# Kernel optimization log

Hardware: AMD Instinct MI355X
Metric: run time of the kernel (lower is better)

The kernel has to match this reference:

```python
import jax, jax.numpy as jnp
import numpy as np

B, S, DIM = 2, 2048, 2048
NH = 16
D_NOPE, D_ROPE, D_V = 128, 64, 128
D_QK = D_NOPE + D_ROPE  # 192
KV_RANK = 512
RMS_EPS = 1e-6


def setup_inputs() -> dict:
    key = jax.random.key(0)
    ks = jax.random.split(key, 8)
    x = jax.random.normal(ks[0], (B, S, DIM), dtype=jnp.float32)
    # rotary freqs as (cos, sin) pairs: [S, D_ROPE//2, 2]
    pos = jnp.arange(S, dtype=jnp.float32)
    inv_freq = 1.0 / (10000.0 ** (jnp.arange(0, D_ROPE, 2, dtype=jnp.float32) / D_ROPE))
    ang = pos[:, None] * inv_freq[None, :]
    freqs_cis = jnp.stack([jnp.cos(ang), jnp.sin(ang)], axis=-1)
    # causal mask [S, S]
    mask = jnp.where(jnp.arange(S)[None, :] > jnp.arange(S)[:, None], -jnp.inf, 0.0).astype(jnp.float32)
    sd = lambda k, shp, fan: jax.random.normal(k, shp, dtype=jnp.float32) * (fan ** -0.5)
    wq = sd(ks[1], (NH * D_QK, DIM), DIM)
    wkv_a = sd(ks[2], (KV_RANK + D_ROPE, DIM), DIM)
    wkv_b = sd(ks[3], (NH * (D_NOPE + D_V), KV_RANK), KV_RANK)
    wo = sd(ks[4], (DIM, NH * D_V), NH * D_V)
    kv_norm_w = jnp.ones((KV_RANK,), dtype=jnp.float32)
    return {"x": x, "start_pos": 0, "freqs_cis": freqs_cis, "mask": mask,
            "wq": wq, "wkv_a": wkv_a, "wkv_b": wkv_b, "wo": wo, "kv_norm_w": kv_norm_w}


def _rope(x, freqs):
    # x: [b, s, h, d] with d even; freqs: [s, d//2, 2] (cos, sin)
    b, s, h, d = x.shape
    xr = x.reshape(b, s, h, d // 2, 2)
    cos = freqs[None, :, None, :, 0]
    sin = freqs[None, :, None, :, 1]
    ye = xr[..., 0] * cos - xr[..., 1] * sin
    yo = xr[..., 0] * sin + xr[..., 1] * cos
    return jnp.stack([ye, yo], axis=-1).reshape(b, s, h, d)


def _rms_norm(x, w):
    var = jnp.mean(jnp.square(x), axis=-1, keepdims=True)
    return x * jax.lax.rsqrt(var + RMS_EPS) * w


def reference(x, start_pos, freqs_cis, mask, wq, wkv_a, wkv_b, wo, kv_norm_w):
    b, s, _ = x.shape
    scale = D_QK ** -0.5
    # query projection -> [b, s, h, d_qk]
    q = jnp.einsum('bsd,ed->bse', x, wq).reshape(b, s, NH, D_QK)
    q_nope, q_pe = q[..., :D_NOPE], q[..., D_NOPE:]
    q_pe = _rope(q_pe, freqs_cis)
    q = jnp.concatenate([q_nope, q_pe], axis=-1)
    # latent kv projection -> [b, s, kv_rank + d_rope]
    kv = jnp.einsum('bsd,ed->bse', x, wkv_a)
    kv_lat, k_pe = kv[..., :KV_RANK], kv[..., KV_RANK:]
    k_pe = _rope(k_pe[:, :, None, :], freqs_cis)  # [b, s, 1, d_rope]
    kv_up = jnp.einsum('bsr,er->bse', _rms_norm(kv_lat, kv_norm_w), wkv_b)
    kv_up = kv_up.reshape(b, s, NH, D_NOPE + D_V)
    k_nope, v = kv_up[..., :D_NOPE], kv_up[..., D_NOPE:]
    k = jnp.concatenate([k_nope, jnp.broadcast_to(k_pe, (b, s, NH, D_ROPE))], axis=-1)
    # start_pos = 0 prefill: cache[:end_pos] == freshly computed k, v
    scores = jnp.einsum('bshd,bthd->bsht', q, k) * scale
    if mask is not None:
        scores = scores + mask[None, :, None, :]
    probs = jax.nn.softmax(scores.astype(jnp.float32), axis=-1).astype(x.dtype)
    out = jnp.einsum('bsht,bthd->bshd', probs, v)
    return jnp.einsum('bse,de->bsd', out.reshape(b, s, NH * D_V), wo)
```

## Files before the change

### kernel.cpp

```cpp
#include <hip/hip_runtime.h>
#include <hip/hip_bf16.h>


typedef __bf16 bf16x8 __attribute__((ext_vector_type(8)));
typedef float  f32x4  __attribute__((ext_vector_type(4)));
typedef float  f32x16 __attribute__((ext_vector_type(16)));
typedef unsigned short us8 __attribute__((ext_vector_type(8)));
typedef unsigned short us4 __attribute__((ext_vector_type(4)));
typedef unsigned int   ui4 __attribute__((ext_vector_type(4)));

#define S_LEN   2048
#define BS_TOT  4096
#define NH      16
#define DQK     192
#define DV      128
#define KV_RANK 512
#define QSTR    3840

__device__ inline unsigned short f2bf(float f) {
  __hip_bfloat16 h = __float2bfloat16(f);
  return *reinterpret_cast<unsigned short*>(&h);
}
__device__ inline float bfu2f(unsigned short u) {
  unsigned int x = ((unsigned int)u) << 16;
  return __builtin_bit_cast(float, x);
}
__device__ inline unsigned int pack2bf(float a, float b) {
  return (unsigned int)f2bf(a) | ((unsigned int)f2bf(b) << 16);
}
__device__ inline void glds16(const void* g, void* l) {
  __builtin_amdgcn_global_load_lds(
      (const __attribute__((address_space(1))) unsigned int*)g,
      (__attribute__((address_space(3))) unsigned int*)l, 16, 0, 0);
}

__global__ __launch_bounds__(256) void cast_all_kernel(
    const float* __restrict__ x, const float* __restrict__ wq,
    const float* __restrict__ wkva, const float* __restrict__ wkvb,
    const float* __restrict__ wo,
    __hip_bfloat16* __restrict__ xb, __hip_bfloat16* __restrict__ wqb,
    __hip_bfloat16* __restrict__ wkvab, __hip_bfloat16* __restrict__ wkvbb,
    __hip_bfloat16* __restrict__ wob) {
  const int bid = blockIdx.x;
  const float* src; __hip_bfloat16* dst; int n, npad, b0, nb;
  if (bid < 771)       { src = x;    dst = xb;    n = 8388608; npad = 8388608; b0 = 0;    nb = 771; }
  else if (bid < 1349) { src = wq;   dst = wqb;   n = 6291456; npad = 6291456; b0 = 771;  nb = 578; }
  else if (bid < 1469) { src = wkva; dst = wkvab; n = 1179648; npad = 1572864; b0 = 1349; nb = 120; }
  else if (bid < 1662) { src = wkvb; dst = wkvbb; n = 2097152; npad = 2097152; b0 = 1469; nb = 193; }
  else                 { src = wo;   dst = wob;   n = 4194304; npad = 4194304; b0 = 1662; nb = 386; }
  const int tid = (bid - b0) * 256 + threadIdx.x;
  const int stride = nb * 256;
  for (int i = tid * 4; i < npad; i += stride * 4) {
    if (i + 3 < n) {
      f32x4 v = *(const f32x4*)(src + i);
      dst[i + 0] = __float2bfloat16(v.x);
      dst[i + 1] = __float2bfloat16(v.y);
      dst[i + 2] = __float2bfloat16(v.z);
      dst[i + 3] = __float2bfloat16(v.w);
    } else {
#pragma unroll
      for (int z = 0; z < 4; z++)
        dst[i + z] = __float2bfloat16((i + z < n) ? src[i + z] : 0.f);
    }
  }
}

template<int OUT_BF16>
__global__ __launch_bounds__(512, 2) void gemm_bt256(
    const __hip_bfloat16* __restrict__ A, const __hip_bfloat16* __restrict__ Bw,
    void* __restrict__ Cp, int M, int N, int K, int nbx) {
  __shared__ alignas(16) unsigned short Asl[2][256 * 64];
  __shared__ alignas(16) unsigned short Bsl[2][256 * 64];

  const int nwg = gridDim.x;
  const int cpx = nwg >> 3;
  const int id  = (blockIdx.x & 7) * cpx + (blockIdx.x >> 3);
  const int bx = id % nbx, by = id / nbx;
  const int m0 = by * 256, n0 = bx * 256;

  const int tid = threadIdx.x, w = tid >> 6, lane = tid & 63;
  const int wr = w >> 2, wc = w & 3;
  const int ml = lane & 15, quad = lane >> 4;
  const int srow = w * 8 + (lane >> 3);
  const int scol = ((lane & 7) ^ (lane >> 3)) * 8;

  const unsigned short* Ag = (const unsigned short*)A + (size_t)(m0 + srow) * K + scol;
  const unsigned short* Bg = (const unsigned short*)Bw + (size_t)(n0 + srow) * K + scol;

  f32x4 acc[8][4];
#pragma unroll
  for (int i = 0; i < 8; i++)
#pragma unroll
    for (int j = 0; j < 4; j++)
#pragma unroll
      for (int e = 0; e < 4; e++) acc[i][j][e] = 0.0f;

  auto stage = [&](int slot, int k0) {
#pragma unroll
    for (int j = 0; j < 4; j++)
      glds16(Ag + (size_t)j * 64 * K + k0, &Asl[slot][(j * 64 + w * 8) * 64]);
#pragma unroll
    for (int j = 0; j < 4; j++)
      glds16(Bg + (size_t)j * 64 * K + k0, &Bsl[slot][(j * 64 + w * 8) * 64]);
  };

  const int nt = K / 64;
  stage(0, 0);
  stage(1, 64);
  asm volatile("s_waitcnt vmcnt(8)" ::: "memory");
  __builtin_amdgcn_s_barrier();
  asm volatile("" ::: "memory");

  int slot = 0;
  for (int t = 0; t < nt; ++t) {
    const unsigned short* As = &Asl[slot][0];
    const unsigned short* Bs = &Bsl[slot][0];

    bf16x8 bfr[2][2][2];
#pragma unroll
    for (int nh = 0; nh < 2; nh++)
#pragma unroll
      for (int nf = 0; nf < 2; nf++) {
        int r = wc * 64 + nh * 32 + nf * 16 + ml;
        const char* rowp = (const char*)&Bs[r * 64];
#pragma unroll
        for (int ks = 0; ks < 2; ks++)
          bfr[nh][nf][ks] =
              *(const bf16x8*)(rowp + ((ks * 64 + quad * 16) ^ ((ml & 7) << 4)));
      }
#pragma unroll
    for (int mh = 0; mh < 2; mh++) {
      bf16x8 af[4][2];
#pragma unroll
      for (int mf = 0; mf < 4; mf++) {
        int r = wr * 128 + mh * 64 + mf * 16 + ml;
        const char* rowp = (const char*)&As[r * 64];
#pragma unroll
        for (int ks = 0; ks < 2; ks++)
          af[mf][ks] =
              *(const bf16x8*)(rowp + ((ks * 64 + quad * 16) ^ ((ml & 7) << 4)));
      }
      __builtin_amdgcn_s_setprio(1);
#pragma unroll
      for (int nh = 0; nh < 2; nh++)
#pragma unroll
        for (int mf = 0; mf < 4; mf++)
#pragma unroll
          for (int nf = 0; nf < 2; nf++)
#pragma unroll
            for (int ks = 0; ks < 2; ks++)
              acc[mh * 4 + mf][nh * 2 + nf] = __builtin_amdgcn_mfma_f32_16x16x32_bf16(
                  af[mf][ks], bfr[nh][nf][ks], acc[mh * 4 + mf][nh * 2 + nf], 0, 0, 0);
      __builtin_amdgcn_s_setprio(0);
    }

    asm volatile("" ::: "memory");
    __builtin_amdgcn_s_barrier();
    asm volatile("" ::: "memory");
    if (t + 2 < nt) {
      stage(slot, (t + 2) * 64);
      asm volatile("s_waitcnt vmcnt(8)" ::: "memory");
    } else {
      asm volatile("s_waitcnt vmcnt(0)" ::: "memory");
    }
    __builtin_amdgcn_s_barrier();
    asm volatile("" ::: "memory");
    slot ^= 1;
  }

#pragma unroll
  for (int mi = 0; mi < 8; mi++) {
#pragma unroll
    for (int ni = 0; ni < 4; ni++) {
      int col = n0 + wc * 64 + ni * 16 + ml;
      int rowb = m0 + wr * 128 + mi * 16 + quad * 4;
#pragma unroll
      for (int j = 0; j < 4; j++) {
        float v = acc[mi][ni][j];
        if (OUT_BF16)
          ((__hip_bfloat16*)Cp)[(size_t)(rowb + j) * N + col] = __float2bfloat16(v);
        else
          ((float*)Cp)[(size_t)(rowb + j) * N + col] = v;
      }
    }
  }
}

__global__ __launch_bounds__(256) void rope_rms_kernel(
    __hip_bfloat16* __restrict__ qkv, const float* __restrict__ w,
    const float* __restrict__ freqs, __hip_bfloat16* __restrict__ latent,
    __hip_bfloat16* __restrict__ kpe_out) {
  int si = blockIdx.x;
  int s  = si & (S_LEN - 1);
  int tid = threadIdx.x;
#pragma unroll
  for (int p = tid; p < NH * 32; p += 256) {
    int h = p >> 5, i = p & 31;
    size_t base = (size_t)si * QSTR + h * DQK + 128 + 2 * i;
    float c  = freqs[s * 64 + 2 * i];
    float sn = freqs[s * 64 + 2 * i + 1];
    float x0 = __bfloat162float(qkv[base]);
    float x1 = __bfloat162float(qkv[base + 1]);
    qkv[base]     = __float2bfloat16(x0 * c - x1 * sn);
    qkv[base + 1] = __float2bfloat16(x0 * sn + x1 * c);
  }
  const unsigned short* row = (const unsigned short*)qkv + (size_t)si * QSTR + 3072;
  float v0 = bfu2f(row[tid]), v1 = bfu2f(row[tid + 256]);
  float ss = v0 * v0 + v1 * v1;
#pragma unroll
  for (int off = 1; off < 64; off <<= 1) ss += __shfl_xor(ss, off, 64);
  __shared__ float red[4];
  if ((tid & 63) == 0) red[tid >> 6] = ss;
  __syncthreads();
  float tot = red[0] + red[1] + red[2] + red[3];
  float r = rsqrtf(tot / 512.0f + 1e-6f);
  latent[(size_t)si * 512 + tid]       = __float2bfloat16(v0 * r * w[tid]);
  latent[(size_t)si * 512 + tid + 256] = __float2bfloat16(v1 * r * w[tid + 256]);
  if (tid < 32) {
    float c  = freqs[s * 64 + 2 * tid];
    float sn = freqs[s * 64 + 2 * tid + 1];
    float x0 = bfu2f(row[512 + 2 * tid]), x1 = bfu2f(row[512 + 2 * tid + 1]);
    kpe_out[(size_t)si * 64 + 2 * tid]     = __float2bfloat16(x0 * c - x1 * sn);
    kpe_out[(size_t)si * 64 + 2 * tid + 1] = __float2bfloat16(x0 * sn + x1 * c);
  }
}

__global__ __launch_bounds__(512, 2) void attn_mfma_kernel(
    const __hip_bfloat16* __restrict__ qb,
    const __hip_bfloat16* __restrict__ kvup,
    const __hip_bfloat16* __restrict__ kpe,
    unsigned short* __restrict__ op0,
    unsigned short* __restrict__ op1,
    float* __restrict__ mlp0,
    float* __restrict__ mlp1) {
  constexpr int KS = 200;
  constexpr int VS = 36;
  __shared__ alignas(16) unsigned short Ks[2][64 * KS];
  __shared__ alignas(16) unsigned int   Vt2[2][128 * VS];

  const int id = blockIdx.x;
  const int x  = id >> 5;
  const int hb = id & 31;
  const int h  = hb >> 1, b = hb & 1;

  const int tid = threadIdx.x, wave = tid >> 6, lane = tid & 63;
  const int l31 = lane & 31, hh = lane >> 5;
  const float qs2 = 0.07216878364870322f * 1.4426950408889634f;

  const int m16 = tid & 15;
  const int hp  = tid >> 4;
  const int vkey = (m16 & 7) << 2;
  const unsigned short* kvbase = (const unsigned short*)kvup;
  const unsigned short* kpbase = (const unsigned short*)kpe;

  int kr_[3], kc_[3];
#pragma unroll
  for (int it = 0; it < 3; it++) {
    int slot = tid + it * 512;
    kr_[it] = slot / 24;
    kc_[it] = slot - kr_[it] * 24;
  }

#pragma unroll 1
  for (int item = 0; item < 2; ++item) {
    const int qt2    = item ? (7 - x) : x;
    const int kstart = item ? (2 * qt2 + 2) : 0;
    const int kend   = kstart + 2 * qt2 + 2;
    const int qwb = qt2 * 256 + wave * 32;
    const int qg  = qwb + l31;

    bf16x8 Qf[12];
    {
      const unsigned short* qrow = (const unsigned short*)qb +
          (size_t)(b * S_LEN + qg) * QSTR + h * DQK;
#pragma unroll
      for (int s = 0; s < 12; s++)
        Qf[s] = *(const bf16x8*)(qrow + s * 16 + hh * 8);
    }

    float m_i = -1e30f, l_i = 0.0f;
    f32x16 O2[4];
#pragma unroll
    for (int mt = 0; mt < 4; mt++)
#pragma unroll
      for (int j = 0; j < 16; j++) O2[mt][j] = 0.0f;

    us8 Kpre[3], Vpre[2];

    const unsigned short* kptr[3];
    int kstep[3];
#pragma unroll
    for (int it = 0; it < 3; it++) {
      if (kc_[it] < 16) {
        kptr[it] = kvbase + (size_t)(b * S_LEN + kstart * 64 + kr_[it]) * (NH * 256)
                   + h * 256 + kc_[it] * 8;
        kstep[it] = 64 * NH * 256;
      } else {
        kptr[it] = kpbase + (size_t)(b * S_LEN + kstart * 64 + kr_[it]) * 64
                   + (kc_[it] - 16) * 8;
        kstep[it] = 64 * 64;
      }
    }
    const unsigned short* vptr = kvbase +
        (size_t)(b * S_LEN + kstart * 64 + 2 * hp) * (NH * 256) + h * 256 + 128 + m16 * 8;

    if (item) __syncthreads();

    {
#pragma unroll
      for (int it = 0; it < 3; it++) {
        Kpre[it] = *(const us8*)kptr[it];
        kptr[it] += kstep[it];
      }
      Vpre[0] = *(const us8*)vptr;
      Vpre[1] = *(const us8*)(vptr + NH * 256);
      vptr += 64 * NH * 256;
#pragma unroll
      for (int it = 0; it < 3; it++)
        *(us8*)&Ks[0][kr_[it] * KS + kc_[it] * 8] = Kpre[it];
#pragma unroll
      for (int z = 0; z < 8; z++) {
        int d = m16 * 8 + z;
        Vt2[0][d * VS + (hp ^ vkey)] =
            (unsigned)(unsigned short)Vpre[0][z] |
            ((unsigned)(unsigned short)Vpre[1][z] << 16);
      }
      __syncthreads();
    }

    int cur = 0;
    for (int kt = kstart; kt < kend; kt++) {
      const int kb = kt * 64;
      const unsigned short* ksc = Ks[cur];
      const unsigned int*   vtc = Vt2[cur];

      const int havenext = (kt + 1 < kend);
      if (havenext) {
#pragma unroll
        for (int it = 0; it < 3; it++) {
          Kpre[it] = *(const us8*)kptr[it];
          kptr[it] += kstep[it];
        }
        Vpre[0] = *(const us8*)vptr;
        Vpre[1] = *(const us8*)(vptr + NH * 256);
        vptr += 64 * NH * 256;
      }

      if (kb <= qwb + 31) {
        f32x16 st2[2];
        __builtin_amdgcn_s_setprio(1);
#pragma unroll
        for (int mt = 0; mt < 2; mt++) {
          f32x16 acc;
#pragma unroll
          for (int j = 0; j < 16; j++) acc[j] = 0.0f;
#pragma unroll
          for (int s = 0; s < 12; s++) {
            bf16x8 kf = *(const bf16x8*)&ksc[(mt * 32 + l31) * KS + s * 16 + hh * 8];
            acc = __builtin_amdgcn_mfma_f32_32x32x16_bf16(kf, Qf[s], acc, 0, 0, 0);
          }
          st2[mt] = acc;
        }
        __builtin_amdgcn_s_setprio(0);

        if (kb + 64 > qwb) {
#pragma unroll
          for (int mt = 0; mt < 2; mt++)
#pragma unroll
            for (int r = 0; r < 16; r++) {
              int kpos = kb + mt * 32 + (r & 3) + 8 * (r >> 2) + 4 * hh;
              st2[mt][r] = (kpos > qg) ? -1e30f : st2[mt][r];
            }
        }
        float t16[16];
#pragma unroll
        for (int r = 0; r < 16; r++) t16[r] = fmaxf(st2[0][r], st2[1][r]);
#pragma unroll
        for (int sw = 8; sw >= 1; sw >>= 1)
#pragma unroll
          for (int r = 0; r < 8; r++)
            if (r < sw) t16[r] = fmaxf(t16[r], t16[r + sw]);
        float mloc = t16[0] * qs2;
        mloc = fmaxf(mloc, __shfl_xor(mloc, 32, 64));
        if (!__all(mloc <= m_i + 8.0f)) {
          float m_new = fmaxf(m_i, mloc);
          float alpha = exp2f(m_i - m_new);
          l_i *= alpha;
#pragma unroll
          for (int mt = 0; mt < 4; mt++)
#pragma unroll
            for (int j = 0; j < 16; j++) O2[mt][j] *= alpha;
          m_i = m_new;
        }
        const float nm = -m_i;
#pragma unroll
        for (int mt = 0; mt < 2; mt++)
#pragma unroll
          for (int r = 0; r < 16; r++) {
            float p = exp2f(fmaf(st2[mt][r], qs2, nm));
            st2[mt][r] = p;
          }
        float s16[16];
#pragma unroll
        for (int r = 0; r < 16; r++) s16[r] = st2[0][r] + st2[1][r];
#pragma unroll
        for (int sw = 8; sw >= 1; sw >>= 1)
#pragma unroll
          for (int r = 0; r < 8; r++)
            if (r < sw) s16[r] += s16[r + sw];
        float psum = s16[0];
        psum += __shfl_xor(psum, 32, 64);
        l_i += psum;

        bf16x8 pf[4];
#pragma unroll
        for (int ss = 0; ss < 4; ss++) {
          const int pmt = ss >> 1, gg = ss & 1;
          unsigned int U0 = pack2bf(st2[pmt][gg * 8 + 0], st2[pmt][gg * 8 + 1]);
          unsigned int U1 = pack2bf(st2[pmt][gg * 8 + 2], st2[pmt][gg * 8 + 3]);
          unsigned int U2 = pack2bf(st2[pmt][gg * 8 + 4], st2[pmt][gg * 8 + 5]);
          unsigned int U3 = pack2bf(st2[pmt][gg * 8 + 6], st2[pmt][gg * 8 + 7]);
          unsigned int E0 = __shfl_xor(hh ? U0 : U2, 32, 64);
          unsigned int E1 = __shfl_xor(hh ? U1 : U3, 32, 64);
          ui4 pd;
          pd.x = hh ? E0 : U0;
          pd.y = hh ? E1 : U1;
          pd.z = hh ? U2 : E0;
          pd.w = hh ? U3 : E1;
          pf[ss] = __builtin_bit_cast(bf16x8, pd);
        }

        __builtin_amdgcn_s_setprio(1);
#pragma unroll
        for (int ss = 0; ss < 4; ss++) {
#pragma unroll
          for (int mt = 0; mt < 4; mt++) {
            int v = mt * 32 + l31;
            const unsigned int* vp =
                &vtc[v * VS + ((ss * 8 + hh * 4) ^ (((v >> 3) & 7) << 2))];
            bf16x8 bv = *(const bf16x8*)vp;
            O2[mt] = __builtin_amdgcn_mfma_f32_32x32x16_bf16(bv, pf[ss], O2[mt],
                                                             0, 0, 0);
          }
        }
        __builtin_amdgcn_s_setprio(0);
      }

      if (havenext) {
#pragma unroll
        for (int it = 0; it < 3; it++)
          *(us8*)&Ks[cur ^ 1][kr_[it] * KS + kc_[it] * 8] = Kpre[it];
#pragma unroll
        for (int z = 0; z < 8; z++) {
          int d = m16 * 8 + z;
          Vt2[cur ^ 1][d * VS + (hp ^ vkey)] =
              (unsigned)(unsigned short)Vpre[0][z] |
              ((unsigned)(unsigned short)Vpre[1][z] << 16);
        }
        __syncthreads();
        cur ^= 1;
      }
    }

    unsigned short* op = item ? op1 : op0;
    float* mlp = item ? mlp1 : mlp0;
    const size_t basep = (size_t)(b * S_LEN + qg) * NH + h;
    unsigned short* orow = op + basep * 128;
#pragma unroll
    for (int mt = 0; mt < 4; mt++) {
#pragma unroll
      for (int g = 0; g < 4; g++) {
        us4 pk;
#pragma unroll
        for (int j = 0; j < 4; j++) pk[j] = f2bf(O2[mt][g * 4 + j]);
        *(us4*)(orow + mt * 32 + g * 8 + hh * 4) = pk;
      }
    }
    if (hh == 0) {
      mlp[basep * 2 + 0] = m_i;
      mlp[basep * 2 + 1] = l_i;
    }
  }
}

__global__ __launch_bounds__(256) void attn_combine_kernel(
    const unsigned short* __restrict__ op0, const unsigned short* __restrict__ op1,
    const float* __restrict__ mlp0, const float* __restrict__ mlp1,
    __hip_bfloat16* __restrict__ attn_out) {
  const int bs = blockIdx.x;
  const int tid = threadIdx.x;
  const int h = tid >> 4, dc = (tid & 15) * 8;
  const size_t basep = (size_t)bs * NH + h;
  const us8 a = *(const us8*)(op0 + basep * 128 + dc);
  const us8 c = *(const us8*)(op1 + basep * 128 + dc);
  const float m0 = mlp0[basep * 2], l0 = mlp0[basep * 2 + 1];
  const float m1 = mlp1[basep * 2], l1 = mlp1[basep * 2 + 1];
  const float m = fmaxf(m0, m1);
  const float a0 = exp2f(m0 - m), a1 = exp2f(m1 - m);
  const float inv = 1.0f / (l0 * a0 + l1 * a1);
  us8 o;
#pragma unroll
  for (int z = 0; z < 8; z++) {
    float v = (bfu2f((unsigned short)a[z]) * a0 +
               bfu2f((unsigned short)c[z]) * a1) * inv;
    o[z] = f2bf(v);
  }
  *(us8*)((unsigned short*)attn_out + (size_t)bs * (NH * DV) + h * DV + dc) = o;
}

extern "C" void kernel_launch(void* const* d_in, const int* in_sizes, int n_in,
                              void* d_out, int out_size, void* d_ws, size_t ws_size,
                              hipStream_t stream) {
  const float* x     = (const float*)d_in[0];
  const float* freqs = (const float*)d_in[2];
  const float* wq    = (const float*)d_in[4];
  const float* wkva  = (const float*)d_in[5];
  const float* wkvb  = (const float*)d_in[6];
  const float* wo    = (const float*)d_in[7];
  const float* kvnw  = (const float*)d_in[8];
  float* out = (float*)d_out;

  char* ws = (char*)d_ws;
  size_t off = 0;
  auto alloc = [&](size_t bytes) {
    void* p = ws + off;
    off += (bytes + 255) & ~(size_t)255;
    return p;
  };
  __hip_bfloat16* x_bf    = (__hip_bfloat16*)alloc((size_t)BS_TOT * 2048 * 2);
  __hip_bfloat16* wq_bf   = (__hip_bfloat16*)alloc((size_t)3072 * 2048 * 2);
  __hip_bfloat16* wkva_bf = (__hip_bfloat16*)alloc((size_t)768 * 2048 * 2);
  __hip_bfloat16* wkvb_bf = (__hip_bfloat16*)alloc((size_t)4096 * 512 * 2);
  __hip_bfloat16* wo_bf   = (__hip_bfloat16*)alloc((size_t)2048 * 2048 * 2);
  __hip_bfloat16* qkv_bf  = (__hip_bfloat16*)alloc((size_t)BS_TOT * QSTR * 2);
  __hip_bfloat16* latent  = (__hip_bfloat16*)alloc((size_t)BS_TOT * 512 * 2);
  __hip_bfloat16* kpe     = (__hip_bfloat16*)alloc((size_t)BS_TOT * 64 * 2);
  __hip_bfloat16* kvup    = (__hip_bfloat16*)alloc((size_t)BS_TOT * 4096 * 2);
  __hip_bfloat16* attn    = (__hip_bfloat16*)alloc((size_t)BS_TOT * 2048 * 2);

  unsigned short* op0 = (unsigned short*)x_bf;
  unsigned short* op1 = (unsigned short*)wq_bf;
  float* mlp0 = (float*)latent;
  float* mlp1 = mlp0 + (size_t)BS_TOT * NH * 2;

  cast_all_kernel<<<2048, 256, 0, stream>>>(x, wq, wkva, wkvb, wo,
                                            x_bf, wq_bf, wkva_bf, wkvb_bf, wo_bf);

  gemm_bt256<1><<<dim3(240), 512, 0, stream>>>(
      x_bf, wq_bf, qkv_bf, BS_TOT, QSTR, 2048, QSTR / 256);
  rope_rms_kernel<<<BS_TOT, 256, 0, stream>>>(qkv_bf, kvnw, freqs, latent, kpe);

  gemm_bt256<1><<<dim3(256), 512, 0, stream>>>(
      latent, wkvb_bf, kvup, BS_TOT, 4096, 512, 16);

  attn_mfma_kernel<<<dim3(256, 1, 1), 512, 0, stream>>>(
      qkv_bf, kvup, kpe, op0, op1, mlp0, mlp1);
  attn_combine_kernel<<<dim3(BS_TOT, 1, 1), 256, 0, stream>>>(
      op0, op1, mlp0, mlp1, attn);

  gemm_bt256<0><<<dim3(128), 512, 0, stream>>>(
      attn, wo_bf, out, BS_TOT, 2048, 2048, 8);
}
```

Baseline: 261.1 us.

## Restructure 256x256 GEMM into four quadrant phases with interleaved half-tile prefetch

Splits the A and B LDS tiles into 128-row halves and walks the 256x256 output tile as four 128x128 quadrants per K-step. Each quadrant phase issues the global-to-LDS load for one half tile, so memory traffic is spread across the compute phases instead of arriving in one burst per K-step. The warp layout changes accordingly, and launch bounds drop to one block per CU. In exchange there are more barriers per K-step and lower occupancy, and the staged-buffer scheme is harder to keep correct.

```diff
diff --git a/kernel.cpp b/kernel.cpp
--- a/kernel.cpp
+++ b/kernel.cpp
@@ -66,11 +66,11 @@
 }
 
 template<int OUT_BF16>
-__global__ __launch_bounds__(512, 2) void gemm_bt256(
+__global__ __launch_bounds__(512, 1) void gemm_bt256(
     const __hip_bfloat16* __restrict__ A, const __hip_bfloat16* __restrict__ Bw,
     void* __restrict__ Cp, int M, int N, int K, int nbx) {
-  __shared__ alignas(16) unsigned short Asl[2][256 * 64];
-  __shared__ alignas(16) unsigned short Bsl[2][256 * 64];
+  __shared__ alignas(16) unsigned short Ah[2][2][128 * 64];
+  __shared__ alignas(16) unsigned short Bh[2][2][128 * 64];
 
   const int nwg = gridDim.x;
   const int cpx = nwg >> 3;
@@ -87,100 +87,115 @@
   const unsigned short* Ag = (const unsigned short*)A + (size_t)(m0 + srow) * K + scol;
   const unsigned short* Bg = (const unsigned short*)Bw + (size_t)(n0 + srow) * K + scol;
 
-  f32x4 acc[8][4];
-#pragma unroll
-  for (int i = 0; i < 8; i++)
-#pragma unroll
-    for (int j = 0; j < 4; j++)
-#pragma unroll
-      for (int e = 0; e < 4; e++) acc[i][j][e] = 0.0f;
-
-  auto stage = [&](int slot, int k0) {
-#pragma unroll
-    for (int j = 0; j < 4; j++)
-      glds16(Ag + (size_t)j * 64 * K + k0, &Asl[slot][(j * 64 + w * 8) * 64]);
-#pragma unroll
-    for (int j = 0; j < 4; j++)
-      glds16(Bg + (size_t)j * 64 * K + k0, &Bsl[slot][(j * 64 + w * 8) * 64]);
+  f32x4 acc[2][2][4][2];
+#pragma unroll
+  for (int a = 0; a < 2; a++)
+#pragma unroll
+    for (int bq = 0; bq < 2; bq++)
+#pragma unroll
+      for (int i = 0; i < 4; i++)
+#pragma unroll
+        for (int j = 0; j < 2; j++)
+#pragma unroll
+          for (int e = 0; e < 4; e++) acc[a][bq][i][j][e] = 0.0f;
+
+  auto stageA = [&](int ha, int par, int k0) {
+#pragma unroll
+    for (int j = 0; j < 2; j++)
+      glds16(Ag + (size_t)(ha * 128 + j * 64) * K + k0,
+             &Ah[ha][par][(j * 64 + w * 8) * 64]);
   };
+  auto stageB = [&](int hb, int par, int k0) {
+#pragma unroll
+    for (int j = 0; j < 2; j++)
+      glds16(Bg + (size_t)(hb * 128 + j * 64) * K + k0,
+             &Bh[hb][par][(j * 64 + w * 8) * 64]);
+  };
 
   const int nt = K / 64;
-  stage(0, 0);
-  stage(1, 64);
-  asm volatile("s_waitcnt vmcnt(8)" ::: "memory");
+  stageA(0, 0, 0); stageB(0, 0, 0); stageA(1, 0, 0); stageB(1, 0, 0);
+  if (nt > 1) { stageA(0, 1, 64); stageB(0, 1, 64); }
+  asm volatile("s_waitcnt vmcnt(4)" ::: "memory");
   __builtin_amdgcn_s_barrier();
   asm volatile("" ::: "memory");
 
-  int slot = 0;
-  for (int t = 0; t < nt; ++t) {
-    const unsigned short* As = &Asl[slot][0];
-    const unsigned short* Bs = &Bsl[slot][0];
-
-    bf16x8 bfr[2][2][2];
-#pragma unroll
-    for (int nh = 0; nh < 2; nh++)
-#pragma unroll
-      for (int nf = 0; nf < 2; nf++) {
-        int r = wc * 64 + nh * 32 + nf * 16 + ml;
-        const char* rowp = (const char*)&Bs[r * 64];
-#pragma unroll
-        for (int ks = 0; ks < 2; ks++)
-          bfr[nh][nf][ks] =
-              *(const bf16x8*)(rowp + ((ks * 64 + quad * 16) ^ ((ml & 7) << 4)));
-      }
-#pragma unroll
-    for (int mh = 0; mh < 2; mh++) {
-      bf16x8 af[4][2];
+  for (int u = 0; u < nt; ++u) {
+    const int P = u & 1;
+#pragma unroll
+    for (int q = 0; q < 4; ++q) {
+      const int ha = q >> 1, hb = q & 1;
+      const unsigned short* As = &Ah[ha][P][0];
+      const unsigned short* Bs = &Bh[hb][P][0];
+
+      bf16x8 af[4][2], bf[2][2];
 #pragma unroll
       for (int mf = 0; mf < 4; mf++) {
-        int r = wr * 128 + mh * 64 + mf * 16 + ml;
+        int r = wr * 64 + mf * 16 + ml;
         const char* rowp = (const char*)&As[r * 64];
 #pragma unroll
         for (int ks = 0; ks < 2; ks++)
           af[mf][ks] =
               *(const bf16x8*)(rowp + ((ks * 64 + quad * 16) ^ ((ml & 7) << 4)));
       }
+#pragma unroll
+      for (int nf = 0; nf < 2; nf++) {
+        int r = wc * 32 + nf * 16 + ml;
+        const char* rowp = (const char*)&Bs[r * 64];
+#pragma unroll
+        for (int ks = 0; ks < 2; ks++)
+          bf[nf][ks] =
+              *(const bf16x8*)(rowp + ((ks * 64 + quad * 16) ^ ((ml & 7) << 4)));
+      }
+
+      if (q == 0) { if (u + 1 < nt) stageA(1, (u + 1) & 1, (u + 1) * 64); }
+      if (q == 1) { if (u + 1 < nt) stageB(1, (u + 1) & 1, (u + 1) * 64); }
+      if (q == 2) { if (u + 2 < nt) stageA(0, P, (u + 2) * 64); }
+      if (q == 3) {
+        if (u + 2 < nt) stageB(0, P, (u + 2) * 64);
+        asm volatile("s_waitcnt vmcnt(4)" ::: "memory");
+      }
+
+      asm volatile("" ::: "memory");
+      __builtin_amdgcn_s_barrier();
+      asm volatile("s_waitcnt lgkmcnt(0)" ::: "memory");
+      __builtin_amdgcn_sched_barrier(0);
+
       __builtin_amdgcn_s_setprio(1);
 #pragma unroll
-      for (int nh = 0; nh < 2; nh++)
-#pragma unroll
-        for (int mf = 0; mf < 4; mf++)
-#pragma unroll
-          for (int nf = 0; nf < 2; nf++)
-#pragma unroll
-            for (int ks = 0; ks < 2; ks++)
-              acc[mh * 4 + mf][nh * 2 + nf] = __builtin_amdgcn_mfma_f32_16x16x32_bf16(
-                  af[mf][ks], bfr[nh][nf][ks], acc[mh * 4 + mf][nh * 2 + nf], 0, 0, 0);
+      for (int mf = 0; mf < 4; mf++)
+#pragma unroll
+        for (int nf = 0; nf < 2; nf++)
+#pragma unroll
+          for (int ks = 0; ks < 2; ks++)
+            acc[ha][hb][mf][nf] = __builtin_amdgcn_mfma_f32_16x16x32_bf16(
+                af[mf][ks], bf[nf][ks], acc[ha][hb][mf][nf], 0, 0, 0);
       __builtin_amdgcn_s_setprio(0);
-    }
-
-    asm volatile("" ::: "memory");
-    __builtin_amdgcn_s_barrier();
-    asm volatile("" ::: "memory");
-    if (t + 2 < nt) {
-      stage(slot, (t + 2) * 64);
-      asm volatile("s_waitcnt vmcnt(8)" ::: "memory");
-    } else {
-      asm volatile("s_waitcnt vmcnt(0)" ::: "memory");
-    }
-    __builtin_amdgcn_s_barrier();
-    asm volatile("" ::: "memory");
-    slot ^= 1;
-  }
-
-#pragma unroll
-  for (int mi = 0; mi < 8; mi++) {
-#pragma unroll
-    for (int ni = 0; ni < 4; ni++) {
-      int col = n0 + wc * 64 + ni * 16 + ml;
-      int rowb = m0 + wr * 128 + mi * 16 + quad * 4;
-#pragma unroll
-      for (int j = 0; j < 4; j++) {
-        float v = acc[mi][ni][j];
-        if (OUT_BF16)
-          ((__hip_bfloat16*)Cp)[(size_t)(rowb + j) * N + col] = __float2bfloat16(v);
-        else
-          ((float*)Cp)[(size_t)(rowb + j) * N + col] = v;
+
+      asm volatile("" ::: "memory");
+      __builtin_amdgcn_s_barrier();
+      asm volatile("" ::: "memory");
+    }
+  }
+
+#pragma unroll
+  for (int ha = 0; ha < 2; ha++) {
+#pragma unroll
+    for (int hb = 0; hb < 2; hb++) {
+#pragma unroll
+      for (int mf = 0; mf < 4; mf++) {
+#pragma unroll
+        for (int nf = 0; nf < 2; nf++) {
+          int col = n0 + hb * 128 + wc * 32 + nf * 16 + ml;
+          int rowb = m0 + ha * 128 + wr * 64 + mf * 16 + quad * 4;
+#pragma unroll
+          for (int j = 0; j < 4; j++) {
+            float v = acc[ha][hb][mf][nf][j];
+            if (OUT_BF16)
+              ((__hip_bfloat16*)Cp)[(size_t)(rowb + j) * N + col] = __float2bfloat16(v);
+            else
+              ((float*)Cp)[(size_t)(rowb + j) * N + col] = v;
+          }
+        }
       }
     }
   }
```

After: 268.9 us. 3.0% more time.
